# Optimization experiments

Hardware: AMD Instinct MI355X
Metric: run time of the kernel (lower is better)

Reference implementation:

```python
import jax, jax.numpy as jnp
import numpy as np
from functools import partial

NF, CD, NB = 64, 32, 3  # num_feat, chan_dyn, num_block


def _conv(x, w, b, stride, pad):
    out = jax.lax.conv_general_dilated(x, w, (stride, stride), ((pad, pad), (pad, pad)),
                                       dimension_numbers=('NCHW', 'OIHW', 'NCHW'))
    return out + b[None, :, None, None]


def _condition_tp(x, w1, b1, w2, b2, w3, b3):
    # ZeroPad2d(1) + conv(stride=2, pad=0) == conv with pad=1, stride=2
    h = jax.nn.relu(_conv(x, w1, b1, 2, 1))   # 7x7
    h = jax.nn.relu(_conv(h, w2, b2, 2, 1))   # 3x3
    h = jax.nn.relu(_conv(h, w3, b3, 2, 1))   # 3x3
    return h.mean(axis=(2, 3))                # [N, 32]


def _lstm_step(x, h, c, w):
    # ConvLSTMCell with 1x1 kernel on 1x1 spatial maps -> plain matmul
    gates = jnp.concatenate([x, h], axis=1) @ w.T        # [N, 4*NF]
    i, f, o, g = jnp.split(gates, 4, axis=1)
    c = jax.nn.sigmoid(f) * c + jax.nn.sigmoid(i) * jnp.tanh(g)
    h = jax.nn.sigmoid(o) * jnp.tanh(c)
    return h, c


def _forward(x, cond, rep_w1, rep_w2, lstm_fw_w, lstm_bw_w, lstm_conv_w, lstm_conv_b,
             conv_first_w, conv_first_b, bc1_w, bc1_b, bc2_w, bc2_b, bc3_w, bc3_b,
             bscale_w, bscale_b, bshift_w, bshift_b, bshare1_w, bshare1_b, bdyn1_w,
             bshare2_w, bshare2_b, bdyn2_w, fc1_w, fc1_b, fc2_w, fc2_b, fc3_w, fc3_b,
             fconv_w, fconv_b, fscale_w, fscale_b, fshift_w, fshift_b):
    lrelu = partial(jax.nn.leaky_relu, negative_slope=0.1)
    b = x.shape[0]
    # conv_represent -> [B, CD*NF] -> pseudo-batch [CD*B, NF] (spatial is 1x1)
    rep = (lrelu(cond @ rep_w1.T) @ rep_w2.T).reshape(b * CD, NF)
    # bidirectional ConvLSTM over 2*NB steps of the same input
    hf = cf = hb = cb = jnp.zeros_like(rep)
    ws_for, ws_back = [], []
    for _ in range(NB * 2):
        hf, cf = _lstm_step(rep, hf, cf, lstm_fw_w)
        ws_for.append(hf)
        hb, cb = _lstm_step(rep, hb, cb, lstm_bw_w)
        ws_back.append(hb)
    ws_back = ws_back[::-1]

    x1 = jnp.einsum('oc,bchw->bohw', conv_first_w, x) + conv_first_b[None, :, None, None]
    for j in range(NB):
        ow1 = (jnp.concatenate([ws_for[2 * j], ws_back[2 * j]], axis=1) @ lstm_conv_w[2 * j].T
               + lstm_conv_b[2 * j]).reshape(b, CD, NF)
        ow2 = (jnp.concatenate([ws_for[2 * j + 1], ws_back[2 * j + 1]], axis=1) @ lstm_conv_w[2 * j + 1].T
               + lstm_conv_b[2 * j + 1]).reshape(b, CD, NF)
        # res_model
        cond_out = _condition_tp(x1, bc1_w[j], bc1_b[j], bc2_w[j], bc2_b[j], bc3_w[j], bc3_b[j])
        scale = (cond_out @ bscale_w[j].T + bscale_b[j])[:, :, None, None]
        shift = (cond_out @ bshift_w[j].T + bshift_b[j])[:, :, None, None]
        # HDA_conv 1: per-sample dynamic 1x1 conv + shared 1x1 conv
        dyn1 = jnp.einsum('oc,boc,bchw->bohw', bdyn1_w[j], ow1, x1)
        share1 = jnp.einsum('oc,bchw->bohw', bshare1_w[j], x1) + bshare1_b[j][None, :, None, None]
        out = jnp.concatenate([dyn1, share1], axis=1)
        out = jax.nn.relu(out * scale + shift + out)
        # HDA_conv 2
        dyn2 = jnp.einsum('oc,boc,bchw->bohw', bdyn2_w[j], ow2, out)
        share2 = jnp.einsum('oc,bchw->bohw', bshare2_w[j], out) + bshare2_b[j][None, :, None, None]
        x1 = x1 + jnp.concatenate([dyn2, share2], axis=1)  # res_scale = 1
    # feature_mo
    cond_out = _condition_tp(x1, fc1_w, fc1_b, fc2_w, fc2_b, fc3_w, fc3_b)
    scale = (cond_out @ fscale_w.T + fscale_b)[:, :, None, None]
    shift = (cond_out @ fshift_w.T + fshift_b)[:, :, None, None]
    out = jnp.einsum('oc,bchw->bohw', fconv_w, x1) + fconv_b[None, :, None, None]
    return out * scale + shift + out


def setup_inputs() -> dict:
    key = jax.random.key(0)
    ctr = iter(range(1000))
    def p(shape, s=0.05):
        return jax.random.normal(jax.random.fold_in(key, next(ctr)), shape, dtype=jnp.float32) * s
    d = {}
    d['x'] = p((2, 3, 384, 640), 1.0)
    d['cond'] = p((2, 7680), 1.0)
    d['rep_w1'] = p((64, 7680)); d['rep_w2'] = p((2048, 64))
    d['lstm_fw_w'] = p((4 * NF, 2 * NF)); d['lstm_bw_w'] = p((4 * NF, 2 * NF))
    d['lstm_conv_w'] = p((2 * NB, NF, 2 * NF)); d['lstm_conv_b'] = p((2 * NB, NF))
    d['conv_first_w'] = p((NF, 3)); d['conv_first_b'] = p((NF,))
    d['bc1_w'] = p((NB, 32, 64, 7, 7)); d['bc1_b'] = p((NB, 32))
    d['bc2_w'] = p((NB, 32, 32, 3, 3)); d['bc2_b'] = p((NB, 32))
    d['bc3_w'] = p((NB, 32, 32, 3, 3)); d['bc3_b'] = p((NB, 32))
    d['bscale_w'] = p((NB, NF, 32)); d['bscale_b'] = p((NB, NF))
    d['bshift_w'] = p((NB, NF, 32)); d['bshift_b'] = p((NB, NF))
    d['bshare1_w'] = p((NB, CD, NF)); d['bshare1_b'] = p((NB, CD))
    d['bdyn1_w'] = p((NB, CD, NF))
    d['bshare2_w'] = p((NB, CD, NF)); d['bshare2_b'] = p((NB, CD))
    d['bdyn2_w'] = p((NB, CD, NF))
    d['fc1_w'] = p((32, 64, 7, 7)); d['fc1_b'] = p((32,))
    d['fc2_w'] = p((32, 32, 3, 3)); d['fc2_b'] = p((32,))
    d['fc3_w'] = p((32, 32, 3, 3)); d['fc3_b'] = p((32,))
    d['fconv_w'] = p((2, NF)); d['fconv_b'] = p((2,))
    d['fscale_w'] = p((2, 32)); d['fscale_b'] = p((2,))
    d['fshift_w'] = p((2, 32)); d['fshift_b'] = p((2,))
    return d


def reference(x, cond, rep_w1, rep_w2, lstm_fw_w, lstm_bw_w, lstm_conv_w, lstm_conv_b,
              conv_first_w, conv_first_b, bc1_w, bc1_b, bc2_w, bc2_b, bc3_w, bc3_b,
              bscale_w, bscale_b, bshift_w, bshift_b, bshare1_w, bshare1_b, bdyn1_w,
              bshare2_w, bshare2_b, bdyn2_w, fc1_w, fc1_b, fc2_w, fc2_b, fc3_w, fc3_b,
              fconv_w, fconv_b, fscale_w, fscale_b, fshift_w, fshift_b):
    return _forward(x, cond, rep_w1, rep_w2, lstm_fw_w, lstm_bw_w, lstm_conv_w, lstm_conv_b,
                    conv_first_w, conv_first_b, bc1_w, bc1_b, bc2_w, bc2_b, bc3_w, bc3_b,
                    bscale_w, bscale_b, bshift_w, bshift_b, bshare1_w, bshare1_b, bdyn1_w,
                    bshare2_w, bshare2_b, bdyn2_w, fc1_w, fc1_b, fc2_w, fc2_b, fc3_w, fc3_b,
                    fconv_w, fconv_b, fscale_w, fscale_b, fshift_w, fshift_b)
```

## Files before the change

kernel.cpp:

```cpp
#include <hip/hip_runtime.h>
#include <math.h>

#define HW 245760
#define H_IN 384
#define W_IN 640

#define X1_OFF   0UL
#define C1_OFF   31457280UL
#define C2_OFF   35324160UL
#define C3_OFF   36290880UL
#define T1_OFF   36536640UL
#define REP_OFF  36536768UL
#define GX_OFF   36540864UL
#define WSF_OFF  36573632UL
#define WSB_OFF  36598208UL
#define OW_OFF   36622784UL
#define CO_OFF   36647360UL
#define PAR_OFF  36647424UL
#define FP_OFF   36664192UL
#define P_W1T 0
#define P_W2T 8192
#define P_B1  16384
#define P_B2  16448
#define P_SC  16512
#define P_SH  16640

#define X1BF_BYTES_OFF 146656800UL
#define X1BF_BYTES     62914560UL
#define WBF_BYTES_OFF  (X1BF_BYTES_OFF + X1BF_BYTES)
#define WBF_BYTES      802816UL
#define REQ_BYTES      (WBF_BYTES_OFF + WBF_BYTES)

typedef short short8 __attribute__((ext_vector_type(8)));
typedef unsigned short ushort8_t __attribute__((ext_vector_type(8)));
typedef unsigned short ushort4_t __attribute__((ext_vector_type(4)));
typedef float f32x16 __attribute__((ext_vector_type(16)));

__device__ __forceinline__ float sigf(float x){ return 1.f/(1.f+expf(-x)); }

__device__ __forceinline__ unsigned short f2bf(float f){
  union { float f; unsigned u; } x; x.f = f;
  unsigned r = x.u + 0x7fffu + ((x.u >> 16) & 1u);
  return (unsigned short)(r >> 16);
}
__device__ __forceinline__ float bf2f(unsigned short u){
  union { unsigned u; float f; } x; x.u = ((unsigned)u) << 16; return x.f;
}

__global__ __launch_bounds__(256) void k_rep1(const float* __restrict__ cond,
                                              const float* __restrict__ w1,
                                              float* __restrict__ ws){
  const int gid = blockIdx.x*256 + threadIdx.x;
  const int o = gid >> 6;
  const int lane = gid & 63;
  const int r = o >> 6, oc = o & 63;
  const float4* c4 = (const float4*)(cond + r*7680);
  const float4* w4 = (const float4*)(w1 + oc*7680);
  float s = 0.f;
  #pragma unroll 6
  for (int i = lane; i < 1920; i += 64){
    float4 a = c4[i], b = w4[i];
    s += a.x*b.x + a.y*b.y + a.z*b.z + a.w*b.w;
  }
  #pragma unroll
  for (int off = 32; off; off >>= 1) s += __shfl_xor(s, off, 64);
  if (lane == 0) ws[T1_OFF + o] = s > 0.f ? s : 0.1f*s;
}

__global__ __launch_bounds__(256) void k_rep2(const float* __restrict__ w2,
                                              float* __restrict__ ws){
  int gid = blockIdx.x*256 + threadIdx.x;
  int r = gid >> 11, j = gid & 2047;
  const float* t1 = ws + T1_OFF + r*64;
  const float* wr = w2 + j*64;
  float s = 0.f;
  #pragma unroll
  for (int k=0;k<64;k++) s += t1[k]*wr[k];
  ws[REP_OFF + gid] = s;
}

__global__ __launch_bounds__(256) void k_gx(const float* __restrict__ wfw,
                                            const float* __restrict__ wbw,
                                            float* __restrict__ ws){
  int gid = blockIdx.x*256 + threadIdx.x;
  int dir = gid >> 14; int rem = gid & 16383;
  int r = rem >> 8; int m = rem & 255;
  const float* w = (dir ? wbw : wfw) + m*128;
  const float* rp = ws + REP_OFF + r*64;
  float s = 0.f;
  #pragma unroll
  for (int k=0;k<64;k++) s += rp[k]*w[k];
  ws[GX_OFF + gid] = s;
}

__global__ __launch_bounds__(256) void k_lstm(const float* __restrict__ wfw,
                                              const float* __restrict__ wbw,
                                              float* __restrict__ ws){
  const int rg = blockIdx.x, dir = blockIdx.y;
  const int tid = threadIdx.x;
  const int gi = tid >> 6, col = tid & 63;
  const float* w = dir ? wbw : wfw;
  const float* gx = ws + GX_OFF + (size_t)dir*16384;
  float* outp = ws + (dir ? WSB_OFF : WSF_OFF);
  float wr[64];
  const float4* wrow = (const float4*)(w + (gi*64+col)*128 + 64);
  #pragma unroll
  for (int k4=0;k4<16;k4++){
    float4 t = wrow[k4];
    wr[k4*4+0]=t.x; wr[k4*4+1]=t.y; wr[k4*4+2]=t.z; wr[k4*4+3]=t.w;
  }
  __shared__ __align__(16) float hl[512];
  __shared__ float gl[2048];
  hl[tid] = 0.f; hl[tid+256] = 0.f;
  float cs0 = 0.f, cs1 = 0.f;
  __syncthreads();
  for (int t=0;t<6;t++){
    float acc[8];
    #pragma unroll
    for (int r=0;r<8;r++) acc[r] = gx[(rg*8+r)*256 + gi*64 + col];
    #pragma unroll
    for (int r=0;r<8;r++){
      #pragma unroll
      for (int k4=0;k4<16;k4++){
        float4 h4 = *(const float4*)&hl[r*64 + k4*4];
        acc[r] += h4.x*wr[k4*4] + h4.y*wr[k4*4+1] + h4.z*wr[k4*4+2] + h4.w*wr[k4*4+3];
      }
    }
    #pragma unroll
    for (int r=0;r<8;r++) gl[r*256 + gi*64 + col] = acc[r];
    __syncthreads();
    {
      int r = tid >> 6, cc = tid & 63;
      float vi = gl[r*256+cc], vf = gl[r*256+64+cc], vo = gl[r*256+128+cc], vg = gl[r*256+192+cc];
      cs0 = sigf(vf)*cs0 + sigf(vi)*tanhf(vg);
      float h = sigf(vo)*tanhf(cs0);
      hl[r*64+cc] = h;
      outp[t*4096 + (rg*8+r)*64 + cc] = h;
    }
    {
      int cid = tid + 256; int r = cid >> 6, cc = cid & 63;
      float vi = gl[r*256+cc], vf = gl[r*256+64+cc], vo = gl[r*256+128+cc], vg = gl[r*256+192+cc];
      cs1 = sigf(vf)*cs1 + sigf(vi)*tanhf(vg);
      float h = sigf(vo)*tanhf(cs1);
      hl[r*64+cc] = h;
      outp[t*4096 + (rg*8+r)*64 + cc] = h;
    }
    __syncthreads();
  }
}

__global__ __launch_bounds__(256) void k_ow(const float* __restrict__ lcw,
                                            const float* __restrict__ lcb,
                                            float* __restrict__ ws){
  int gid = blockIdx.x*256 + threadIdx.x;
  int t = gid >> 12; int rem = gid & 4095;
  int r = rem >> 6; int cc = rem & 63;
  const float* wf = lcw + t*8192 + cc*128;
  const float* xf = ws + WSF_OFF + t*4096 + r*64;
  const float* xb = ws + WSB_OFF + (size_t)(5-t)*4096 + r*64;
  float s = lcb[t*64+cc];
  #pragma unroll
  for (int k=0;k<64;k++) s += xf[k]*wf[k];
  #pragma unroll
  for (int k=0;k<64;k++) s += xb[k]*wf[64+k];
  ws[OW_OFF + gid] = s;
}

__global__ __launch_bounds__(256) void k_convfirst(const float* __restrict__ x,
                                                   const float* __restrict__ cw,
                                                   const float* __restrict__ cb,
                                                   float* __restrict__ x1planar,
                                                   unsigned short* __restrict__ xbf){
  __shared__ float wsm[192];
  __shared__ float bsm[64];
  const int tid = threadIdx.x, blk = blockIdx.x;
  const int b = blk / 960;
  const int px = (blk % 960)*256 + tid;
  if (tid < 192) wsm[tid] = cw[tid];
  if (tid < 64)  bsm[tid] = cb[tid];
  __syncthreads();
  float x0 = x[(size_t)(b*3+0)*HW + px];
  float x1v = x[(size_t)(b*3+1)*HW + px];
  float x2 = x[(size_t)(b*3+2)*HW + px];
  float* o = x1planar ? (x1planar + (size_t)b*64*HW + px) : (float*)0;
  #pragma unroll
  for (int i=0;i<8;i++){
    ushort8_t u;
    #pragma unroll
    for (int j=0;j<8;j++){
      int oc = i*8+j;
      float v = bsm[oc] + wsm[oc*3]*x0 + wsm[oc*3+1]*x1v + wsm[oc*3+2]*x2;
      if (x1planar) o[(size_t)oc*HW] = v;
      u[j] = f2bf(v);
    }
    if (xbf)
      *(ushort8_t*)(xbf + (((size_t)(i>>1)*2 + b)*HW + px)*16 + (i&1)*8) = u;
  }
}

__global__ __launch_bounds__(256) void k_wbf(const float* __restrict__ bc1w,
                                             const float* __restrict__ fc1w,
                                             unsigned short* __restrict__ wbf){
  int e = blockIdx.x*256 + threadIdx.x;
  int s = e / 100352; int r = e - s*100352;
  int tap = r >> 11; int rem = r & 2047; int oc = rem >> 6; int ic = rem & 63;
  const float* src = (s < 3) ? (bc1w + (size_t)s*100352) : fc1w;
  wbf[e] = f2bf(src[((size_t)oc*64 + ic)*49 + tap]);
}

__global__ __launch_bounds__(512, 2) void k_conv7_mfma(
    const unsigned short* __restrict__ xbf,
    const unsigned short* __restrict__ wbf,
    const float* __restrict__ bias,
    float* __restrict__ out)
{
  __shared__ __align__(16) unsigned short inS[37*2*36*16];
  __shared__ __align__(16) unsigned short wS[49*32*16];
  const int tid = threadIdx.x;
  const int wv = tid >> 6, l = tid & 63;
  const int mrow = l & 31, khalf = l >> 5;
  const int wo0 = blockIdx.x * 32, ho0 = blockIdx.y * 16;
  const int b = blockIdx.z;
  const int r0 = 2*ho0 - 1;

  f32x16 acc0, acc1;
  #pragma unroll
  for (int i=0;i<16;i++){ acc0[i]=0.f; acc1[i]=0.f; }

  for (int kc = 0; kc < 4; ++kc){
    const unsigned short* xplane = xbf + ((size_t)(kc*2 + b))*HW*16;
    __syncthreads();
    for (int idx = tid; idx < 37*72*2; idx += 512){
      int half = idx & 1; int e = idx >> 1;
      int row = e / 72; int rem = e - row*72;
      int p = (rem >= 36) ? 1 : 0;
      int qi = rem - 36*p;
      int r = r0 + row;
      int col = 2*(qi + wo0 - 1) + p;
      uint4 v = make_uint4(0u,0u,0u,0u);
      if ((unsigned)r < 384u && (unsigned)col < 640u)
        v = *(const uint4*)(xplane + ((size_t)r*640 + col)*16 + half*8);
      *(uint4*)(inS + ((size_t)e*16 + half*8)) = v;
    }
    for (int idx = tid; idx < 49*32*2; idx += 512){
      int half = idx & 1; int e = idx >> 1;
      uint4 v = *(const uint4*)(wbf + ((size_t)e*64 + kc*16 + half*8));
      *(uint4*)(wS + ((size_t)e*16 + half*8)) = v;
    }
    __syncthreads();
    #pragma unroll
    for (int kh = 0; kh < 7; ++kh){
      short8 Bf[7];
      #pragma unroll
      for (int kw = 0; kw < 7; ++kw)
        Bf[kw] = *(const short8*)(wS + (((kh*7+kw)*32 + mrow)*16 + khalf*8));
      const int ra = 4*wv + kh;
      #pragma unroll
      for (int kw = 0; kw < 7; ++kw){
        const int p = (kw+1)&1;
        const int qoff = (kw - 1 - p)/2 + 1;
        short8 A0 = *(const short8*)(inS + ((((ra)*2 + p)*36 + qoff + mrow)*16 + khalf*8));
        acc0 = __builtin_amdgcn_mfma_f32_32x32x16_bf16(A0, Bf[kw], acc0, 0, 0, 0);
        short8 A1 = *(const short8*)(inS + ((((ra+2)*2 + p)*36 + qoff + mrow)*16 + khalf*8));
        acc1 = __builtin_amdgcn_mfma_f32_32x32x16_bf16(A1, Bf[kw], acc1, 0, 0, 0);
      }
    }
  }

  const float bv = bias[mrow];
  #pragma unroll
  for (int mt = 0; mt < 2; ++mt){
    int ho = ho0 + 2*wv + mt;
    if (ho >= 190) continue;
    f32x16 av = mt ? acc1 : acc0;
    float* orow = out + (((size_t)b*32 + mrow)*190 + ho)*318;
    #pragma unroll
    for (int r = 0; r < 16; ++r){
      int m = (r&3) + 8*(r>>2) + 4*khalf;
      int wo = wo0 + m;
      if (wo < 318) orow[wo] = fmaxf(av[r] + bv, 0.f);
    }
  }
}

__global__ __launch_bounds__(256) void k_conv7(const float* __restrict__ in,
                                               const float* __restrict__ w,
                                               const float* __restrict__ bias,
                                               float* __restrict__ out){
  __shared__ float patch[37*37];
  __shared__ __align__(16) float wl[49*32];
  const int tid = threadIdx.x;
  const int og = tid >> 5, s = tid & 31;
  const int sy = s >> 1, sx0 = (s & 1)*8;
  const int bx = blockIdx.x, by = blockIdx.y, b = blockIdx.z;
  const int ir0 = by*32 - 1, ic0 = bx*32 - 1;
  float acc[4][8];
  #pragma unroll
  for (int i=0;i<4;i++)
    #pragma unroll
    for (int k=0;k<8;k++) acc[i][k]=0.f;
  for (int c=0;c<64;c++){
    const float* src = in + (size_t)(b*64+c)*HW;
    for (int idx=tid; idx<1369; idx+=256){
      int r = idx/37; int cc = idx - r*37;
      int ir = ir0 + r, ic = ic0 + cc;
      float v = 0.f;
      if ((unsigned)ir < H_IN && (unsigned)ic < W_IN) v = src[ir*W_IN + ic];
      patch[idx] = v;
    }
    for (int idx=tid; idx<1568; idx+=256)
      wl[idx] = w[((size_t)(idx&31)*64 + c)*49 + (idx>>5)];
    __syncthreads();
    #pragma unroll
    for (int kh=0;kh<7;kh++){
      const float* prow = &patch[(2*sy+kh)*37 + 2*sx0];
      #pragma unroll
      for (int kw=0;kw<7;kw++){
        float4 wv = *(const float4*)&wl[(kh*7+kw)*32 + og*4];
        #pragma unroll
        for (int i=0;i<8;i++){
          float xv = prow[2*i + kw];
          acc[0][i] += wv.x*xv; acc[1][i] += wv.y*xv;
          acc[2][i] += wv.z*xv; acc[3][i] += wv.w*xv;
        }
      }
    }
    __syncthreads();
  }
  const int ho = by*16 + sy;
  if (ho < 190){
    #pragma unroll
    for (int oo=0;oo<4;oo++){
      int o = og*4+oo; float bb = bias[o];
      float* orow = out + ((size_t)(b*32+o)*190 + ho)*318 + bx*16 + sx0;
      #pragma unroll
      for (int i=0;i<8;i++){
        int wo = bx*16 + sx0 + i;
        if (wo < 318) orow[i] = fmaxf(acc[oo][i] + bb, 0.f);
      }
    }
  }
}

__global__ __launch_bounds__(256) void k_conv3_fast(const float* __restrict__ in,
                                                    const float* __restrict__ w,
                                                    const float* __restrict__ bias,
                                                    float* __restrict__ out,
                                                    int Hi, int Wi, int Ho, int Wo){
  __shared__ __align__(16) float wl[32*9*8];
  const int tid = threadIdx.x;
  const int b = blockIdx.z;
  const int oc0 = blockIdx.y * 8;
  for (int idx = tid; idx < 2304; idx += 256){
    int ol = idx & 7; int rest = idx >> 3;
    int ic = rest / 9, k = rest - ic*9;
    wl[idx] = w[((size_t)(oc0+ol)*32 + ic)*9 + k];
  }
  __syncthreads();
  const int pxl = tid & 127, ocg = tid >> 7;
  const int HoWo = Ho*Wo;
  const int opx = blockIdx.x*128 + pxl;
  if (opx >= HoWo) return;
  const int ho = opx / Wo, wo = opx - ho*Wo;
  const int ir0 = 2*ho - 1, ic0 = 2*wo - 1;
  const float* inb = in + (size_t)b*32*Hi*Wi;
  float acc0=0.f, acc1=0.f, acc2=0.f, acc3=0.f;
  for (int c = 0; c < 32; ++c){
    const float* src = inb + (size_t)c*Hi*Wi;
    float xv[9];
    #pragma unroll
    for (int kh=0;kh<3;kh++){
      int ir = ir0 + kh;
      bool rok = (unsigned)ir < (unsigned)Hi;
      #pragma unroll
      for (int kw=0;kw<3;kw++){
        int icc = ic0 + kw;
        xv[kh*3+kw] = (rok && (unsigned)icc < (unsigned)Wi) ? src[ir*Wi + icc] : 0.f;
      }
    }
    const float* wc = &wl[c*72 + ocg*4];
    #pragma unroll
    for (int k=0;k<9;k++){
      float4 wa = *(const float4*)(wc + k*8);
      float x = xv[k];
      acc0 += wa.x*x; acc1 += wa.y*x; acc2 += wa.z*x; acc3 += wa.w*x;
    }
  }
  float* ob = out + ((size_t)(b*32 + oc0 + ocg*4))*HoWo + opx;
  acc0 = fmaxf(acc0 + bias[oc0+ocg*4+0], 0.f);
  acc1 = fmaxf(acc1 + bias[oc0+ocg*4+1], 0.f);
  acc2 = fmaxf(acc2 + bias[oc0+ocg*4+2], 0.f);
  acc3 = fmaxf(acc3 + bias[oc0+ocg*4+3], 0.f);
  ob[0] = acc0;
  ob[(size_t)HoWo] = acc1;
  ob[(size_t)2*HoWo] = acc2;
  ob[(size_t)3*HoWo] = acc3;
}

__global__ __launch_bounds__(256) void k_mean(float* __restrict__ ws){
  __shared__ float red[256];
  const float* p = ws + C3_OFF + (size_t)blockIdx.x*3840;
  float s = 0.f;
  for (int i=threadIdx.x; i<3840; i+=256) s += p[i];
  red[threadIdx.x] = s;
  __syncthreads();
  for (int st=128; st>0; st>>=1){
    if (threadIdx.x < st) red[threadIdx.x] += red[threadIdx.x+st];
    __syncthreads();
  }
  if (threadIdx.x == 0) ws[CO_OFF + blockIdx.x] = red[0]*(1.f/3840.f);
}

__global__ __launch_bounds__(256) void k_mkparams(const float* __restrict__ bsw, const float* __restrict__ bsb,
                                                  const float* __restrict__ bhw, const float* __restrict__ bhb,
                                                  const float* __restrict__ dyn1, const float* __restrict__ sh1w, const float* __restrict__ sh1b,
                                                  const float* __restrict__ dyn2, const float* __restrict__ sh2w, const float* __restrict__ sh2b,
                                                  int j2, float* __restrict__ ws,
                                                  unsigned short* __restrict__ w1oc,
                                                  unsigned short* __restrict__ w2oc){
  const float* co = ws + CO_OFF;
  const float* ow1 = ws + OW_OFF + (size_t)j2*4096;
  const float* ow2 = ws + OW_OFF + (size_t)(j2+1)*4096;
  float* P = ws + PAR_OFF;
  const int tid = threadIdx.x;
  if (tid < 128){
    int b = tid>>6, o = tid&63;
    float s = bsb[o];
    #pragma unroll
    for (int k=0;k<32;k++) s += co[b*32+k]*bsw[o*32+k];
    P[P_SC + tid] = 1.f + s;
  } else {
    int t2 = tid-128; int b = t2>>6, o = t2&63;
    float s = bhb[o];
    #pragma unroll
    for (int k=0;k<32;k++) s += co[b*32+k]*bhw[o*32+k];
    P[P_SH + t2] = s;
  }
  for (int idx=tid; idx<8192; idx+=256){
    int b = idx>>12, rem = idx&4095, c = rem>>6, o = rem&63;
    float v1, v2;
    if (o < 32){
      v1 = dyn1[o*64+c]*ow1[(b*32+o)*64+c];
      v2 = dyn2[o*64+c]*ow2[(b*32+o)*64+c];
    } else {
      v1 = sh1w[(o-32)*64+c];
      v2 = sh2w[(o-32)*64+c];
    }
    P[P_W1T + idx] = v1;
    P[P_W2T + idx] = v2;
    int t = b*4096 + o*64 + c;
    w1oc[t] = f2bf(v1);
    w2oc[t] = f2bf(v2);
  }
  if (tid < 64){
    P[P_B1+tid] = (tid<32) ? 0.f : sh1b[tid-32];
    P[P_B2+tid] = (tid<32) ? 0.f : sh2b[tid-32];
  }
}

__global__ __launch_bounds__(256, 3) void k_pointwise_mfma(
    const float* __restrict__ ws,
    const unsigned short* __restrict__ w1oc,
    const unsigned short* __restrict__ w2oc,
    unsigned short* __restrict__ xbf)
{
  __shared__ float scs[64], shs[64], b1s[64], b2s[64];
  __shared__ __align__(16) uint4 outbuf[2048];
  const int tid = threadIdx.x;
  const int blk = blockIdx.x;
  const int b = blk / 960;
  const int px0 = (blk % 960) * 256;
  const float* P = ws + PAR_OFF;
  if (tid < 64){
    scs[tid] = P[P_SC + b*64 + tid];
    shs[tid] = P[P_SH + b*64 + tid];
    b1s[tid] = P[P_B1 + tid];
    b2s[tid] = P[P_B2 + tid];
  }
  __syncthreads();
  const int wv = tid >> 6, l = tid & 63;
  const int lane31 = l & 31, myh = l >> 5;
  const unsigned short* w1g = w1oc + (size_t)b*4096;
  const unsigned short* w2g = w2oc + (size_t)b*4096;

  #pragma unroll
  for (int nt = 0; nt < 2; ++nt){
    const int pxl = wv*64 + nt*32 + lane31;
    const int mypx = px0 + pxl;
    short8 Bsave[4];
    f32x16 a1_0, a1_1;
    #pragma unroll
    for (int i=0;i<16;i++){ a1_0[i]=0.f; a1_1[i]=0.f; }
    #pragma unroll
    for (int kc=0;kc<4;kc++){
      short8 Bx = *(const short8*)(xbf + ((size_t)(kc*2+b)*HW + mypx)*16 + myh*8);
      Bsave[kc] = Bx;
      short8 A0 = *(const short8*)(w1g + (size_t)lane31*64 + kc*16 + myh*8);
      short8 A1 = *(const short8*)(w1g + (size_t)(32+lane31)*64 + kc*16 + myh*8);
      a1_0 = __builtin_amdgcn_mfma_f32_32x32x16_bf16(A0, Bx, a1_0, 0, 0, 0);
      a1_1 = __builtin_amdgcn_mfma_f32_32x32x16_bf16(A1, Bx, a1_1, 0, 0, 0);
    }
    unsigned hp0[8], hp1[8];
    #pragma unroll
    for (int mt=0;mt<2;mt++){
      #pragma unroll
      for (int p=0;p<8;p++){
        unsigned half0=0, half1=0;
        #pragma unroll
        for (int e=0;e<2;e++){
          int reg = 2*p+e;
          int o1 = mt*32 + (reg&3) + 8*(reg>>2) + 4*myh;
          float v = mt ? a1_1[reg] : a1_0[reg];
          float t = (v + b1s[o1]) * scs[o1] + shs[o1];
          t = fmaxf(t, 0.f);
          if (e) half1 = f2bf(t); else half0 = f2bf(t);
        }
        unsigned pk = half0 | (half1<<16);
        if (mt) hp1[p] = pk; else hp0[p] = pk;
      }
    }
    f32x16 a2_0, a2_1;
    #pragma unroll
    for (int i=0;i<16;i++){ a2_0[i]=0.f; a2_1[i]=0.f; }
    #pragma unroll
    for (int kc=0;kc<4;kc++){
      const int base = 4*(kc&1);
      unsigned e0,e1,e2,e3;
      if (kc < 2){ e0=hp0[base+0]; e1=hp0[base+1]; e2=hp0[base+2]; e3=hp0[base+3]; }
      else       { e0=hp1[base+0]; e1=hp1[base+1]; e2=hp1[base+2]; e3=hp1[base+3]; }
      unsigned sA = myh ? e0 : e2;
      unsigned sB = myh ? e1 : e3;
      unsigned rA = __shfl_xor(sA, 32, 64);
      unsigned rB = __shfl_xor(sB, 32, 64);
      union { unsigned u[4]; short8 s; } Bh;
      Bh.u[0] = myh ? rA : e0;
      Bh.u[1] = myh ? rB : e1;
      Bh.u[2] = myh ? e2 : rA;
      Bh.u[3] = myh ? e3 : rB;
      short8 A0 = *(const short8*)(w2g + (size_t)lane31*64 + kc*16 + myh*8);
      short8 A1 = *(const short8*)(w2g + (size_t)(32+lane31)*64 + kc*16 + myh*8);
      a2_0 = __builtin_amdgcn_mfma_f32_32x32x16_bf16(A0, Bh.s, a2_0, 0, 0, 0);
      a2_1 = __builtin_amdgcn_mfma_f32_32x32x16_bf16(A1, Bh.s, a2_1, 0, 0, 0);
    }
    #pragma unroll
    for (int mt2=0;mt2<2;mt2++){
      #pragma unroll
      for (int q=0;q<4;q++){
        float d[4], p[4];
        #pragma unroll
        for (int e=0;e<4;e++){
          int reg = 4*q+e;
          int ch = mt2*32 + e + 8*q + 4*myh;
          d[e] = (mt2 ? a2_1[reg] : a2_0[reg]) + b2s[ch];
        }
        #pragma unroll
        for (int e=0;e<4;e++) p[e] = __shfl_xor(d[e], 32, 64);
        if (myh == (q & 1)){
          float row8[8];
          #pragma unroll
          for (int e=0;e<4;e++){
            row8[e]   = myh ? p[e] : d[e];
            row8[4+e] = myh ? d[e] : p[e];
          }
          union { short8 s; unsigned short us[8]; } oldv;
          oldv.s = Bsave[2*mt2 + (q>>1)];
          unsigned w[4];
          #pragma unroll
          for (int k=0;k<4;k++){
            float n0 = bf2f(oldv.us[2*k+0]) + row8[2*k+0];
            float n1 = bf2f(oldv.us[2*k+1]) + row8[2*k+1];
            w[k] = (unsigned)f2bf(n0) | ((unsigned)f2bf(n1) << 16);
          }
          int slot = mt2*4 + q;
          outbuf[pxl*8 + ((slot + pxl) & 7)] = make_uint4(w[0],w[1],w[2],w[3]);
        }
      }
    }
  }
  __syncthreads();
  uint4* gout = (uint4*)xbf;
  #pragma unroll
  for (int k=0;k<8;k++){
    int idx = tid + k*256;
    int plane = idx >> 9, rem = idx & 511;
    int pxl = rem >> 1, half = rem & 1;
    int slot = plane*2 + half;
    gout[((size_t)(plane*2+b)*HW + px0 + pxl)*2 + half] = outbuf[pxl*8 + ((slot + pxl) & 7)];
  }
}

#define FMA4(A,W,X) { A.x += (W)*(X).x; A.y += (W)*(X).y; A.z += (W)*(X).z; A.w += (W)*(X).w; }
__global__ __launch_bounds__(128) void k_pointwise(float* __restrict__ ws){
  __shared__ __align__(16) float xt[64*128];
  __shared__ __align__(16) float wt[64*64];
  __shared__ float b1s[64], b2s[64], scs[64], shs[64];
  const int tid = threadIdx.x;
  const int blk = blockIdx.x;
  const int b = blk / 1920;
  const int px0 = (blk % 1920) * 128;
  float* x1 = ws + X1_OFF;
  const float* P = ws + PAR_OFF;
  const float4* xg = (const float4*)(x1 + (size_t)b*64*HW + px0);
  float4* xt4 = (float4*)xt;
  float4* wt4 = (float4*)wt;
  for (int idx=tid; idx<2048; idx+=128){
    int c = idx>>5, p4 = idx&31;
    xt4[c*32 + (p4&3)*8 + (p4>>2)] = xg[(size_t)c*(HW/4) + p4];
  }
  const float4* w1g = (const float4*)(P + P_W1T + b*4096);
  for (int idx=tid; idx<1024; idx+=128) wt4[idx] = w1g[idx];
  if (tid < 64){
    b1s[tid]=P[P_B1+tid]; b2s[tid]=P[P_B2+tid];
    scs[tid]=P[P_SC + b*64 + tid]; shs[tid]=P[P_SH + b*64 + tid];
  }
  __syncthreads();
  const int og = tid>>3, pg = tid&7, o0 = og*4;
  float4 a[4][4];
  #pragma unroll
  for (int oo=0;oo<4;oo++){
    float bv = b1s[o0+oo];
    a[oo][0]=a[oo][1]=a[oo][2]=a[oo][3]=make_float4(bv,bv,bv,bv);
  }
  for (int c=0;c<64;c++){
    float4 wv = wt4[c*16 + og];
    float4 x0 = xt4[c*32 + pg];
    float4 x1q = xt4[c*32 + 8 + pg];
    float4 x2 = xt4[c*32 + 16 + pg];
    float4 x3 = xt4[c*32 + 24 + pg];
    FMA4(a[0][0],wv.x,x0); FMA4(a[0][1],wv.x,x1q); FMA4(a[0][2],wv.x,x2); FMA4(a[0][3],wv.x,x3);
    FMA4(a[1][0],wv.y,x0); FMA4(a[1][1],wv.y,x1q); FMA4(a[1][2],wv.y,x2); FMA4(a[1][3],wv.y,x3);
    FMA4(a[2][0],wv.z,x0); FMA4(a[2][1],wv.z,x1q); FMA4(a[2][2],wv.z,x2); FMA4(a[2][3],wv.z,x3);
    FMA4(a[3][0],wv.w,x0); FMA4(a[3][1],wv.w,x1q); FMA4(a[3][2],wv.w,x2); FMA4(a[3][3],wv.w,x3);
  }
  #pragma unroll
  for (int oo=0;oo<4;oo++){
    float sc = scs[o0+oo], sh = shs[o0+oo];
    #pragma unroll
    for (int q=0;q<4;q++){
      a[oo][q].x = fmaxf(a[oo][q].x*sc + sh, 0.f);
      a[oo][q].y = fmaxf(a[oo][q].y*sc + sh, 0.f);
      a[oo][q].z = fmaxf(a[oo][q].z*sc + sh, 0.f);
      a[oo][q].w = fmaxf(a[oo][q].w*sc + sh, 0.f);
    }
  }
  __syncthreads();
  #pragma unroll
  for (int oo=0;oo<4;oo++)
    #pragma unroll
    for (int q=0;q<4;q++)
      xt4[(o0+oo)*32 + q*8 + pg] = a[oo][q];
  const float4* w2g = (const float4*)(P + P_W2T + b*4096);
  for (int idx=tid; idx<1024; idx+=128) wt4[idx] = w2g[idx];
  __syncthreads();
  #pragma unroll
  for (int oo=0;oo<4;oo++){
    float bv = b2s[o0+oo];
    a[oo][0]=a[oo][1]=a[oo][2]=a[oo][3]=make_float4(bv,bv,bv,bv);
  }
  for (int c=0;c<64;c++){
    float4 wv = wt4[c*16 + og];
    float4 x0 = xt4[c*32 + pg];
    float4 x1q = xt4[c*32 + 8 + pg];
    float4 x2 = xt4[c*32 + 16 + pg];
    float4 x3 = xt4[c*32 + 24 + pg];
    FMA4(a[0][0],wv.x,x0); FMA4(a[0][1],wv.x,x1q); FMA4(a[0][2],wv.x,x2); FMA4(a[0][3],wv.x,x3);
    FMA4(a[1][0],wv.y,x0); FMA4(a[1][1],wv.y,x1q); FMA4(a[1][2],wv.y,x2); FMA4(a[1][3],wv.y,x3);
    FMA4(a[2][0],wv.z,x0); FMA4(a[2][1],wv.z,x1q); FMA4(a[2][2],wv.z,x2); FMA4(a[2][3],wv.z,x3);
    FMA4(a[3][0],wv.w,x0); FMA4(a[3][1],wv.w,x1q); FMA4(a[3][2],wv.w,x2); FMA4(a[3][3],wv.w,x3);
  }
  #pragma unroll
  for (int q=0;q<4;q++){
    #pragma unroll
    for (int oo=0;oo<4;oo++){
      float4* xo = (float4*)(x1 + (size_t)(b*64 + o0+oo)*HW + px0);
      float4 old = xo[pg*4 + q];
      old.x += a[oo][q].x; old.y += a[oo][q].y; old.z += a[oo][q].z; old.w += a[oo][q].w;
      xo[pg*4 + q] = old;
    }
  }
}

__global__ void k_mkfinal(const float* __restrict__ fsw, const float* __restrict__ fsb,
                          const float* __restrict__ fhw, const float* __restrict__ fhb,
                          float* __restrict__ ws){
  int tid = threadIdx.x;
  if (tid < 4){
    int b = tid>>1, o = tid&1;
    const float* co = ws + CO_OFF + b*32;
    float s = fsb[o], h = fhb[o];
    for (int k=0;k<32;k++){ s += co[k]*fsw[o*32+k]; h += co[k]*fhw[o*32+k]; }
    ws[FP_OFF + tid] = 1.f + s;
    ws[FP_OFF + 4 + tid] = h;
  }
}

__global__ __launch_bounds__(256) void k_final_bf(const float* __restrict__ fw,
                                                  const float* __restrict__ fb,
                                                  const float* __restrict__ ws,
                                                  const unsigned short* __restrict__ xbf,
                                                  float* __restrict__ out){
  __shared__ float w[128];
  __shared__ float pr[8];
  __shared__ float bb[2];
  const int tid = threadIdx.x, blk = blockIdx.x;
  const int b = blk / 960;
  const int px = (blk % 960)*256 + tid;
  if (tid < 128) w[tid] = fw[tid];
  if (tid < 8)   pr[tid] = ws[FP_OFF + tid];
  if (tid < 2)   bb[tid] = fb[tid];
  __syncthreads();
  float a0 = bb[0], a1 = bb[1];
  #pragma unroll
  for (int p=0;p<4;p++){
    const unsigned short* row = xbf + ((size_t)(p*2+b)*HW + px)*16;
    #pragma unroll
    for (int hh=0;hh<2;hh++){
      union { uint4 v; unsigned short us[8]; } u;
      u.v = *(const uint4*)(row + hh*8);
      #pragma unroll
      for (int j=0;j<8;j++){
        int c = p*16 + hh*8 + j;
        float f = bf2f(u.us[j]);
        a0 += w[c]*f; a1 += w[64+c]*f;
      }
    }
  }
  out[((size_t)b*2+0)*HW + px] = a0*pr[b*2+0] + pr[4 + b*2+0];
  out[((size_t)b*2+1)*HW + px] = a1*pr[b*2+1] + pr[4 + b*2+1];
}

__global__ __launch_bounds__(256) void k_final(const float* __restrict__ fw,
                                               const float* __restrict__ fb,
                                               const float* __restrict__ ws,
                                               float* __restrict__ out){
  __shared__ float w[128];
  __shared__ float pr[8];
  __shared__ float bb[2];
  const int tid = threadIdx.x, blk = blockIdx.x;
  const int b = blk / 960;
  const int px = (blk % 960)*256 + tid;
  if (tid < 128) w[tid] = fw[tid];
  if (tid < 8)   pr[tid] = ws[FP_OFF + tid];
  if (tid < 2)   bb[tid] = fb[tid];
  __syncthreads();
  const float* xp = ws + X1_OFF + (size_t)b*64*HW + px;
  float a0 = bb[0], a1 = bb[1];
  #pragma unroll
  for (int c=0;c<64;c++){
    float xv = xp[(size_t)c*HW];
    a0 += w[c]*xv; a1 += w[64+c]*xv;
  }
  out[((size_t)b*2+0)*HW + px] = a0*pr[b*2+0] + pr[4 + b*2+0];
  out[((size_t)b*2+1)*HW + px] = a1*pr[b*2+1] + pr[4 + b*2+1];
}

extern "C" void kernel_launch(void* const* d_in, const int* in_sizes, int n_in,
                              void* d_out, int out_size, void* d_ws, size_t ws_size,
                              hipStream_t stream) {
  const float* x            = (const float*)d_in[0];
  const float* cond         = (const float*)d_in[1];
  const float* rep_w1       = (const float*)d_in[2];
  const float* rep_w2       = (const float*)d_in[3];
  const float* lstm_fw_w    = (const float*)d_in[4];
  const float* lstm_bw_w    = (const float*)d_in[5];
  const float* lstm_conv_w  = (const float*)d_in[6];
  const float* lstm_conv_b  = (const float*)d_in[7];
  const float* conv_first_w = (const float*)d_in[8];
  const float* conv_first_b = (const float*)d_in[9];
  const float* bc1_w  = (const float*)d_in[10];
  const float* bc1_b  = (const float*)d_in[11];
  const float* bc2_w  = (const float*)d_in[12];
  const float* bc2_b  = (const float*)d_in[13];
  const float* bc3_w  = (const float*)d_in[14];
  const float* bc3_b  = (const float*)d_in[15];
  const float* bscale_w = (const float*)d_in[16];
  const float* bscale_b = (const float*)d_in[17];
  const float* bshift_w = (const float*)d_in[18];
  const float* bshift_b = (const float*)d_in[19];
  const float* bshare1_w = (const float*)d_in[20];
  const float* bshare1_b = (const float*)d_in[21];
  const float* bdyn1_w   = (const float*)d_in[22];
  const float* bshare2_w = (const float*)d_in[23];
  const float* bshare2_b = (const float*)d_in[24];
  const float* bdyn2_w   = (const float*)d_in[25];
  const float* fc1_w = (const float*)d_in[26];
  const float* fc1_b = (const float*)d_in[27];
  const float* fc2_w = (const float*)d_in[28];
  const float* fc2_b = (const float*)d_in[29];
  const float* fc3_w = (const float*)d_in[30];
  const float* fc3_b = (const float*)d_in[31];
  const float* fconv_w  = (const float*)d_in[32];
  const float* fconv_b  = (const float*)d_in[33];
  const float* fscale_w = (const float*)d_in[34];
  const float* fscale_b = (const float*)d_in[35];
  const float* fshift_w = (const float*)d_in[36];
  const float* fshift_b = (const float*)d_in[37];

  float* ws = (float*)d_ws;
  const bool use_mfma = (ws_size >= REQ_BYTES);
  unsigned short* xbf = use_mfma ? (unsigned short*)((char*)d_ws + X1BF_BYTES_OFF) : (unsigned short*)0;
  unsigned short* wbf = (unsigned short*)((char*)d_ws + WBF_BYTES_OFF);
  unsigned short* w1oc = (unsigned short*)((char*)d_ws + C1_OFF*4UL);
  unsigned short* w2oc = w1oc + 8192;

  k_rep1<<<32, 256, 0, stream>>>(cond, rep_w1, ws);
  k_rep2<<<16, 256, 0, stream>>>(rep_w2, ws);
  k_gx<<<128, 256, 0, stream>>>(lstm_fw_w, lstm_bw_w, ws);
  k_lstm<<<dim3(8,2), 256, 0, stream>>>(lstm_fw_w, lstm_bw_w, ws);
  k_ow<<<96, 256, 0, stream>>>(lstm_conv_w, lstm_conv_b, ws);
  if (use_mfma)
    k_wbf<<<1568, 256, 0, stream>>>(bc1_w, fc1_w, wbf);
  k_convfirst<<<1920, 256, 0, stream>>>(x, conv_first_w, conv_first_b,
                                        use_mfma ? (float*)0 : (ws + X1_OFF), xbf);

  for (int j = 0; j < 3; j++){
    if (use_mfma){
      k_conv7_mfma<<<dim3(10,12,2), 512, 0, stream>>>(xbf, wbf + (size_t)j*100352, bc1_b + j*32, ws + C1_OFF);
    } else {
      k_conv7<<<dim3(20,12,2), 256, 0, stream>>>(ws + X1_OFF, bc1_w + (size_t)j*32*64*49, bc1_b + j*32, ws + C1_OFF);
    }
    k_conv3_fast<<<dim3(119,4,2), 256, 0, stream>>>(ws + C1_OFF, bc2_w + (size_t)j*32*32*9, bc2_b + j*32, ws + C2_OFF, 190, 318, 95, 159);
    k_conv3_fast<<<dim3(30,4,2), 256, 0, stream>>>(ws + C2_OFF, bc3_w + (size_t)j*32*32*9, bc3_b + j*32, ws + C3_OFF, 95, 159, 48, 80);
    k_mean<<<64, 256, 0, stream>>>(ws);
    k_mkparams<<<1, 256, 0, stream>>>(bscale_w + j*2048, bscale_b + j*64,
                                      bshift_w + j*2048, bshift_b + j*64,
                                      bdyn1_w + j*2048, bshare1_w + j*2048, bshare1_b + j*32,
                                      bdyn2_w + j*2048, bshare2_w + j*2048, bshare2_b + j*32,
                                      2*j, ws, w1oc, w2oc);
    if (use_mfma)
      k_pointwise_mfma<<<1920, 256, 0, stream>>>(ws, w1oc, w2oc, xbf);
    else
      k_pointwise<<<3840, 128, 0, stream>>>(ws);
  }

  if (use_mfma){
    k_conv7_mfma<<<dim3(10,12,2), 512, 0, stream>>>(xbf, wbf + (size_t)3*100352, fc1_b, ws + C1_OFF);
  } else {
    k_conv7<<<dim3(20,12,2), 256, 0, stream>>>(ws + X1_OFF, fc1_w, fc1_b, ws + C1_OFF);
  }
  k_conv3_fast<<<dim3(119,4,2), 256, 0, stream>>>(ws + C1_OFF, fc2_w, fc2_b, ws + C2_OFF, 190, 318, 95, 159);
  k_conv3_fast<<<dim3(30,4,2), 256, 0, stream>>>(ws + C2_OFF, fc3_w, fc3_b, ws + C3_OFF, 95, 159, 48, 80);
  k_mean<<<64, 256, 0, stream>>>(ws);
  k_mkfinal<<<1, 64, 0, stream>>>(fscale_w, fscale_b, fshift_w, fshift_b, ws);
  if (use_mfma)
    k_final_bf<<<1920, 256, 0, stream>>>(fconv_w, fconv_b, ws, xbf, (float*)d_out);
  else
    k_final<<<1920, 256, 0, stream>>>(fconv_w, fconv_b, ws, (float*)d_out);
}
```

Measured before the change: 772.0 us.

## Prefetch conv7 tiles into registers, swizzle LDS, fuse spatial mean into conv3

The 7x7 MFMA conv now loads the next input-channel chunk from global memory into registers while the current chunk is computed. It writes that chunk to LDS through an XOR swizzle meant to cut bank conflicts. Separately, the last stride-2 conv3 no longer stores its output and instead writes per-block channel partial sums through wave shuffles, and mkparams/mkfinal reduce those partials, which removes the k_mean launch. The prefetch adds register pressure under launch bounds of 512 threads with 2 blocks per CU, and the partials reuse the GX workspace region.

```diff
diff --git a/kernel.cpp b/kernel.cpp
--- a/kernel.cpp
+++ b/kernel.cpp
@@ -33,7 +33,6 @@
 
 typedef short short8 __attribute__((ext_vector_type(8)));
 typedef unsigned short ushort8_t __attribute__((ext_vector_type(8)));
-typedef unsigned short ushort4_t __attribute__((ext_vector_type(4)));
 typedef float f32x16 __attribute__((ext_vector_type(16)));
 
 __device__ __forceinline__ float sigf(float x){ return 1.f/(1.f+expf(-x)); }
@@ -208,6 +207,7 @@
   wbf[e] = f2bf(src[((size_t)oc*64 + ic)*49 + tap]);
 }
 
+#define SWZ(b) ((b) ^ ((((b)>>7)&1u)<<4))
 __global__ __launch_bounds__(512, 2) void k_conv7_mfma(
     const unsigned short* __restrict__ xbf,
     const unsigned short* __restrict__ wbf,
@@ -216,6 +216,8 @@
 {
   __shared__ __align__(16) unsigned short inS[37*2*36*16];
   __shared__ __align__(16) unsigned short wS[49*32*16];
+  char* inB = (char*)inS;
+  char* wB  = (char*)wS;
   const int tid = threadIdx.x;
   const int wv = tid >> 6, l = tid & 63;
   const int mrow = l & 31, khalf = l >> 5;
@@ -227,44 +229,83 @@
   #pragma unroll
   for (int i=0;i<16;i++){ acc0[i]=0.f; acc1[i]=0.f; }
 
+  uint4 rin[11]; uint4 rw[7];
+
+  auto LOADI = [&](int kc){
+    const unsigned short* xplane = xbf + ((size_t)(kc*2 + b))*HW*16;
+    #pragma unroll
+    for (int k=0;k<11;k++){
+      int idx = tid + k*512;
+      uint4 v = make_uint4(0u,0u,0u,0u);
+      if (idx < 5328){
+        int half = idx & 1; int e = idx >> 1;
+        int row = e / 72; int rem = e - row*72;
+        int p = (rem >= 36) ? 1 : 0;
+        int qi = rem - 36*p;
+        int r = r0 + row;
+        int col = 2*(qi + wo0 - 1) + p;
+        if ((unsigned)r < 384u && (unsigned)col < 640u)
+          v = *(const uint4*)(xplane + ((size_t)r*640 + col)*16 + half*8);
+      }
+      rin[k] = v;
+    }
+    #pragma unroll
+    for (int k=0;k<7;k++){
+      int idx = tid + k*512;
+      if (idx < 3136){
+        int half = idx & 1; int e = idx >> 1;
+        rw[k] = *(const uint4*)(wbf + ((size_t)e*64 + kc*16 + half*8));
+      }
+    }
+  };
+  auto WRITEI = [&](){
+    #pragma unroll
+    for (int k=0;k<11;k++){
+      int idx = tid + k*512;
+      if (idx < 5328){
+        unsigned bo = SWZ((unsigned)(idx>>1)*32u + (unsigned)(idx&1)*16u);
+        *(uint4*)(inB + bo) = rin[k];
+      }
+    }
+    #pragma unroll
+    for (int k=0;k<7;k++){
+      int idx = tid + k*512;
+      if (idx < 3136){
+        unsigned bo = SWZ((unsigned)(idx>>1)*32u + (unsigned)(idx&1)*16u);
+        *(uint4*)(wB + bo) = rw[k];
+      }
+    }
+  };
+
+  LOADI(0);
+  WRITEI();
+  __syncthreads();
+
   for (int kc = 0; kc < 4; ++kc){
-    const unsigned short* xplane = xbf + ((size_t)(kc*2 + b))*HW*16;
-    __syncthreads();
-    for (int idx = tid; idx < 37*72*2; idx += 512){
-      int half = idx & 1; int e = idx >> 1;
-      int row = e / 72; int rem = e - row*72;
-      int p = (rem >= 36) ? 1 : 0;
-      int qi = rem - 36*p;
-      int r = r0 + row;
-      int col = 2*(qi + wo0 - 1) + p;
-      uint4 v = make_uint4(0u,0u,0u,0u);
-      if ((unsigned)r < 384u && (unsigned)col < 640u)
-        v = *(const uint4*)(xplane + ((size_t)r*640 + col)*16 + half*8);
-      *(uint4*)(inS + ((size_t)e*16 + half*8)) = v;
-    }
-    for (int idx = tid; idx < 49*32*2; idx += 512){
-      int half = idx & 1; int e = idx >> 1;
-      uint4 v = *(const uint4*)(wbf + ((size_t)e*64 + kc*16 + half*8));
-      *(uint4*)(wS + ((size_t)e*16 + half*8)) = v;
-    }
-    __syncthreads();
+    if (kc < 3) LOADI(kc+1);
     #pragma unroll
     for (int kh = 0; kh < 7; ++kh){
       short8 Bf[7];
       #pragma unroll
-      for (int kw = 0; kw < 7; ++kw)
-        Bf[kw] = *(const short8*)(wS + (((kh*7+kw)*32 + mrow)*16 + khalf*8));
+      for (int kw = 0; kw < 7; ++kw){
+        unsigned bo = SWZ(((unsigned)((kh*7+kw)*32 + mrow))*32u + (unsigned)khalf*16u);
+        Bf[kw] = *(const short8*)(wB + bo);
+      }
       const int ra = 4*wv + kh;
       #pragma unroll
       for (int kw = 0; kw < 7; ++kw){
         const int p = (kw+1)&1;
         const int qoff = (kw - 1 - p)/2 + 1;
-        short8 A0 = *(const short8*)(inS + ((((ra)*2 + p)*36 + qoff + mrow)*16 + khalf*8));
+        unsigned bo0 = SWZ(((unsigned)(((ra)*2 + p)*36 + qoff + mrow))*32u + (unsigned)khalf*16u);
+        short8 A0 = *(const short8*)(inB + bo0);
         acc0 = __builtin_amdgcn_mfma_f32_32x32x16_bf16(A0, Bf[kw], acc0, 0, 0, 0);
-        short8 A1 = *(const short8*)(inS + ((((ra+2)*2 + p)*36 + qoff + mrow)*16 + khalf*8));
+        unsigned bo1 = SWZ(((unsigned)(((ra+2)*2 + p)*36 + qoff + mrow))*32u + (unsigned)khalf*16u);
+        short8 A1 = *(const short8*)(inB + bo1);
         acc1 = __builtin_amdgcn_mfma_f32_32x32x16_bf16(A1, Bf[kw], acc1, 0, 0, 0);
       }
     }
+    __syncthreads();
+    if (kc < 3){ WRITEI(); __syncthreads(); }
   }
 
   const float bv = bias[mrow];
@@ -346,8 +387,10 @@
                                                     const float* __restrict__ w,
                                                     const float* __restrict__ bias,
                                                     float* __restrict__ out,
-                                                    int Hi, int Wi, int Ho, int Wo){
+                                                    int Hi, int Wi, int Ho, int Wo,
+                                                    float* __restrict__ co_partial){
   __shared__ __align__(16) float wl[32*9*8];
+  __shared__ float wsum[4][4];
   const int tid = threadIdx.x;
   const int b = blockIdx.z;
   const int oc0 = blockIdx.y * 8;
@@ -360,55 +403,64 @@
   const int pxl = tid & 127, ocg = tid >> 7;
   const int HoWo = Ho*Wo;
   const int opx = blockIdx.x*128 + pxl;
-  if (opx >= HoWo) return;
-  const int ho = opx / Wo, wo = opx - ho*Wo;
-  const int ir0 = 2*ho - 1, ic0 = 2*wo - 1;
-  const float* inb = in + (size_t)b*32*Hi*Wi;
   float acc0=0.f, acc1=0.f, acc2=0.f, acc3=0.f;
-  for (int c = 0; c < 32; ++c){
-    const float* src = inb + (size_t)c*Hi*Wi;
-    float xv[9];
-    #pragma unroll
-    for (int kh=0;kh<3;kh++){
-      int ir = ir0 + kh;
-      bool rok = (unsigned)ir < (unsigned)Hi;
+  if (opx < HoWo){
+    const int ho = opx / Wo, wo = opx - ho*Wo;
+    const int ir0 = 2*ho - 1, ic0 = 2*wo - 1;
+    const float* inb = in + (size_t)b*32*Hi*Wi;
+    for (int c = 0; c < 32; ++c){
+      const float* src = inb + (size_t)c*Hi*Wi;
+      float xv[9];
       #pragma unroll
-      for (int kw=0;kw<3;kw++){
-        int icc = ic0 + kw;
-        xv[kh*3+kw] = (rok && (unsigned)icc < (unsigned)Wi) ? src[ir*Wi + icc] : 0.f;
-      }
-    }
-    const float* wc = &wl[c*72 + ocg*4];
-    #pragma unroll
-    for (int k=0;k<9;k++){
-      float4 wa = *(const float4*)(wc + k*8);
-      float x = xv[k];
-      acc0 += wa.x*x; acc1 += wa.y*x; acc2 += wa.z*x; acc3 += wa.w*x;
-    }
-  }
-  float* ob = out + ((size_t)(b*32 + oc0 + ocg*4))*HoWo + opx;
-  acc0 = fmaxf(acc0 + bias[oc0+ocg*4+0], 0.f);
-  acc1 = fmaxf(acc1 + bias[oc0+ocg*4+1], 0.f);
-  acc2 = fmaxf(acc2 + bias[oc0+ocg*4+2], 0.f);
-  acc3 = fmaxf(acc3 + bias[oc0+ocg*4+3], 0.f);
-  ob[0] = acc0;
-  ob[(size_t)HoWo] = acc1;
-  ob[(size_t)2*HoWo] = acc2;
-  ob[(size_t)3*HoWo] = acc3;
-}
-
-__global__ __launch_bounds__(256) void k_mean(float* __restrict__ ws){
-  __shared__ float red[256];
-  const float* p = ws + C3_OFF + (size_t)blockIdx.x*3840;
-  float s = 0.f;
-  for (int i=threadIdx.x; i<3840; i+=256) s += p[i];
-  red[threadIdx.x] = s;
-  __syncthreads();
-  for (int st=128; st>0; st>>=1){
-    if (threadIdx.x < st) red[threadIdx.x] += red[threadIdx.x+st];
+      for (int kh=0;kh<3;kh++){
+        int ir = ir0 + kh;
+        bool rok = (unsigned)ir < (unsigned)Hi;
+        #pragma unroll
+        for (int kw=0;kw<3;kw++){
+          int icc = ic0 + kw;
+          xv[kh*3+kw] = (rok && (unsigned)icc < (unsigned)Wi) ? src[ir*Wi + icc] : 0.f;
+        }
+      }
+      const float* wc = &wl[c*72 + ocg*4];
+      #pragma unroll
+      for (int k=0;k<9;k++){
+        float4 wa = *(const float4*)(wc + k*8);
+        float x = xv[k];
+        acc0 += wa.x*x; acc1 += wa.y*x; acc2 += wa.z*x; acc3 += wa.w*x;
+      }
+    }
+    acc0 = fmaxf(acc0 + bias[oc0+ocg*4+0], 0.f);
+    acc1 = fmaxf(acc1 + bias[oc0+ocg*4+1], 0.f);
+    acc2 = fmaxf(acc2 + bias[oc0+ocg*4+2], 0.f);
+    acc3 = fmaxf(acc3 + bias[oc0+ocg*4+3], 0.f);
+    if (!co_partial){
+      float* ob = out + ((size_t)(b*32 + oc0 + ocg*4))*HoWo + opx;
+      ob[0] = acc0;
+      ob[(size_t)HoWo] = acc1;
+      ob[(size_t)2*HoWo] = acc2;
+      ob[(size_t)3*HoWo] = acc3;
+    }
+  }
+  if (co_partial){
+    float r0=acc0, r1=acc1, r2=acc2, r3=acc3;
+    #pragma unroll
+    for (int off=32; off; off>>=1){
+      r0 += __shfl_xor(r0, off, 64);
+      r1 += __shfl_xor(r1, off, 64);
+      r2 += __shfl_xor(r2, off, 64);
+      r3 += __shfl_xor(r3, off, 64);
+    }
+    int wvid = tid >> 6;
+    if ((tid & 63) == 0){
+      wsum[wvid][0]=r0; wsum[wvid][1]=r1; wsum[wvid][2]=r2; wsum[wvid][3]=r3;
+    }
     __syncthreads();
-  }
-  if (threadIdx.x == 0) ws[CO_OFF + blockIdx.x] = red[0]*(1.f/3840.f);
+    if (tid < 8){
+      int i = tid & 3; int pair = tid >> 2;
+      float v = wsum[pair*2][i] + wsum[pair*2+1][i];
+      co_partial[(size_t)blockIdx.x*64 + b*32 + oc0 + pair*4 + i] = v;
+    }
+  }
 }
 
 __global__ __launch_bounds__(256) void k_mkparams(const float* __restrict__ bsw, const float* __restrict__ bsb,
@@ -418,22 +470,29 @@
                                                   int j2, float* __restrict__ ws,
                                                   unsigned short* __restrict__ w1oc,
                                                   unsigned short* __restrict__ w2oc){
-  const float* co = ws + CO_OFF;
+  __shared__ float coL[64];
+  const float* part = ws + GX_OFF;
   const float* ow1 = ws + OW_OFF + (size_t)j2*4096;
   const float* ow2 = ws + OW_OFF + (size_t)(j2+1)*4096;
   float* P = ws + PAR_OFF;
   const int tid = threadIdx.x;
+  if (tid < 64){
+    float s = 0.f;
+    for (int bx=0;bx<30;bx++) s += part[bx*64 + tid];
+    coL[tid] = s * (1.f/3840.f);
+  }
+  __syncthreads();
   if (tid < 128){
     int b = tid>>6, o = tid&63;
     float s = bsb[o];
     #pragma unroll
-    for (int k=0;k<32;k++) s += co[b*32+k]*bsw[o*32+k];
+    for (int k=0;k<32;k++) s += coL[b*32+k]*bsw[o*32+k];
     P[P_SC + tid] = 1.f + s;
   } else {
     int t2 = tid-128; int b = t2>>6, o = t2&63;
     float s = bhb[o];
     #pragma unroll
-    for (int k=0;k<32;k++) s += co[b*32+k]*bhw[o*32+k];
+    for (int k=0;k<32;k++) s += coL[b*32+k]*bhw[o*32+k];
     P[P_SH + t2] = s;
   }
   for (int idx=tid; idx<8192; idx+=256){
@@ -683,10 +742,18 @@
 __global__ void k_mkfinal(const float* __restrict__ fsw, const float* __restrict__ fsb,
                           const float* __restrict__ fhw, const float* __restrict__ fhb,
                           float* __restrict__ ws){
+  __shared__ float coL[64];
+  const float* part = ws + GX_OFF;
   int tid = threadIdx.x;
+  if (tid < 64){
+    float s = 0.f;
+    for (int bx=0;bx<30;bx++) s += part[bx*64 + tid];
+    coL[tid] = s * (1.f/3840.f);
+  }
+  __syncthreads();
   if (tid < 4){
     int b = tid>>1, o = tid&1;
-    const float* co = ws + CO_OFF + b*32;
+    const float* co = coL + b*32;
     float s = fsb[o], h = fhb[o];
     for (int k=0;k<32;k++){ s += co[k]*fsw[o*32+k]; h += co[k]*fhw[o*32+k]; }
     ws[FP_OFF + tid] = 1.f + s;
@@ -802,6 +869,7 @@
   unsigned short* wbf = (unsigned short*)((char*)d_ws + WBF_BYTES_OFF);
   unsigned short* w1oc = (unsigned short*)((char*)d_ws + C1_OFF*4UL);
   unsigned short* w2oc = w1oc + 8192;
+  float* copart = ws + GX_OFF;
 
   k_rep1<<<32, 256, 0, stream>>>(cond, rep_w1, ws);
   k_rep2<<<16, 256, 0, stream>>>(rep_w2, ws);
@@ -819,9 +887,8 @@
     } else {
       k_conv7<<<dim3(20,12,2), 256, 0, stream>>>(ws + X1_OFF, bc1_w + (size_t)j*32*64*49, bc1_b + j*32, ws + C1_OFF);
     }
-    k_conv3_fast<<<dim3(119,4,2), 256, 0, stream>>>(ws + C1_OFF, bc2_w + (size_t)j*32*32*9, bc2_b + j*32, ws + C2_OFF, 190, 318, 95, 159);
-    k_conv3_fast<<<dim3(30,4,2), 256, 0, stream>>>(ws + C2_OFF, bc3_w + (size_t)j*32*32*9, bc3_b + j*32, ws + C3_OFF, 95, 159, 48, 80);
-    k_mean<<<64, 256, 0, stream>>>(ws);
+    k_conv3_fast<<<dim3(119,4,2), 256, 0, stream>>>(ws + C1_OFF, bc2_w + (size_t)j*32*32*9, bc2_b + j*32, ws + C2_OFF, 190, 318, 95, 159, (float*)0);
+    k_conv3_fast<<<dim3(30,4,2), 256, 0, stream>>>(ws + C2_OFF, bc3_w + (size_t)j*32*32*9, bc3_b + j*32, ws + C3_OFF, 95, 159, 48, 80, copart);
     k_mkparams<<<1, 256, 0, stream>>>(bscale_w + j*2048, bscale_b + j*64,
                                       bshift_w + j*2048, bshift_b + j*64,
                                       bdyn1_w + j*2048, bshare1_w + j*2048, bshare1_b + j*32,
@@ -838,9 +905,8 @@
   } else {
     k_conv7<<<dim3(20,12,2), 256, 0, stream>>>(ws + X1_OFF, fc1_w, fc1_b, ws + C1_OFF);
   }
-  k_conv3_fast<<<dim3(119,4,2), 256, 0, stream>>>(ws + C1_OFF, fc2_w, fc2_b, ws + C2_OFF, 190, 318, 95, 159);
-  k_conv3_fast<<<dim3(30,4,2), 256, 0, stream>>>(ws + C2_OFF, fc3_w, fc3_b, ws + C3_OFF, 95, 159, 48, 80);
-  k_mean<<<64, 256, 0, stream>>>(ws);
+  k_conv3_fast<<<dim3(119,4,2), 256, 0, stream>>>(ws + C1_OFF, fc2_w, fc2_b, ws + C2_OFF, 190, 318, 95, 159, (float*)0);
+  k_conv3_fast<<<dim3(30,4,2), 256, 0, stream>>>(ws + C2_OFF, fc3_w, fc3_b, ws + C3_OFF, 95, 159, 48, 80, copart);
   k_mkfinal<<<1, 64, 0, stream>>>(fscale_w, fscale_b, fshift_w, fshift_b, ws);
   if (use_mfma)
     k_final_bf<<<1920, 256, 0, stream>>>(fconv_w, fconv_b, ws, xbf, (float*)d_out);
```

Measured after the change: 889.0 us. +15.1%, slower.
